# Kernel tuning notes

Measured on AMD Instinct MI355X. Metric: run time of the kernel, lower is better.

The kernel has to match this reference:

```python
import math
import jax, jax.numpy as jnp
import numpy as np

D_MODEL = 128
NUM_HEADS = 8
FACTOR = 5


def setup_inputs() -> dict:
    key = jax.random.key(0)
    ks = jax.random.split(key, 9)
    B, L, dm = 2, 4096, D_MODEL
    s = 1.0 / math.sqrt(dm)
    return {
        "x": jax.random.normal(ks[0], (B, L, dm), dtype=jnp.float32),
        "Wq": jax.random.normal(ks[1], (dm, dm), dtype=jnp.float32) * s,
        "bq": jnp.zeros((dm,), jnp.float32),
        "Wk": jax.random.normal(ks[2], (dm, dm), dtype=jnp.float32) * s,
        "bk": jnp.zeros((dm,), jnp.float32),
        "Wv": jax.random.normal(ks[3], (dm, dm), dtype=jnp.float32) * s,
        "bv": jnp.zeros((dm,), jnp.float32),
        "Wo": jax.random.normal(ks[4], (dm, dm), dtype=jnp.float32) * s,
        "bo": jnp.zeros((dm,), jnp.float32),
    }


def reference(x, Wq, bq, Wk, bk, Wv, bv, Wo, bo):
    B, L, dm = x.shape
    H = NUM_HEADS
    D = dm // H
    inv_sqrt_d = 1.0 / math.sqrt(D)

    def split_heads(t):  # [B,L,dm] -> [B,H,L,D]
        return t.reshape(B, L, H, D).transpose(0, 2, 1, 3)

    Q = split_heads(x @ Wq + bq)
    K = split_heads(x @ Wk + bk)
    V = split_heads(x @ Wv + bv)

    # sample_k = min(L_K, int(log(L_K) * factor)); L is static under jit
    sample_k = min(L, int(math.log(L) * FACTOR))

    # _prob_QK: full scores, per-query stable exp, mean over queries, top-k keys
    scores_full = jnp.einsum("bhqd,bhkd->bhqk", Q, K) * inv_sqrt_d  # [B,H,L,L]
    m = jnp.max(scores_full, axis=-1, keepdims=True)
    e = jnp.exp(scores_full - m)
    mean_attn = jnp.mean(e, axis=2)  # [B,H,L_K]
    _, idx = jax.lax.top_k(mean_attn, sample_k)  # [B,H,sample_k]

    # gather sampled keys/values along the key axis
    Ks = jnp.take_along_axis(K, idx[..., None], axis=2)  # [B,H,s,D]
    Vs = jnp.take_along_axis(V, idx[..., None], axis=2)

    attn = jax.nn.softmax(jnp.einsum("bhqd,bhsd->bhqs", Q, Ks) * inv_sqrt_d, axis=-1)
    out = jnp.einsum("bhqs,bhsd->bhqd", attn, Vs)  # [B,H,L,D]
    out = out.transpose(0, 2, 1, 3).reshape(B, L, dm)
    return out @ Wo + bo
```

## Files before the change

kernel.cpp:

```cpp
#include <hip/hip_runtime.h>
#include <hip/hip_bf16.h>

#define L 4096
#define DM 128
#define NH 8
#define HD 16
#define NBH 16
#define SK 41
#define NSPLIT 8
#define SLICE (L/NSPLIT)
#define KK (SLICE/16)
#define QSCALE 0.36067376022224085f

typedef __attribute__((ext_vector_type(8))) short s16x8;
typedef __attribute__((ext_vector_type(4))) float f32x4;

#define MFMA16(A,B,C) __builtin_amdgcn_mfma_f32_16x16x32_bf16(A,B,C,0,0,0)

__device__ __forceinline__ float bf2f(unsigned short h){ return __uint_as_float(((unsigned)h)<<16); }
__device__ __forceinline__ unsigned short f2bf(float f){
  unsigned u = __float_as_uint(f);
  u += 0x7FFFu + ((u>>16)&1u);
  return (unsigned short)(u>>16);
}
__device__ __forceinline__ float fast_exp2(float x){
  float r;
  asm("v_exp_f32 %0, %1" : "=v"(r) : "v"(x));
  return r;
}

__global__ __launch_bounds__(256) void prep(
    const float* __restrict__ x,
    const float* __restrict__ Wq, const float* __restrict__ Wk,
    const float* __restrict__ Wv, const float* __restrict__ Wo,
    unsigned short* __restrict__ Xh, unsigned short* __restrict__ Xl,
    unsigned short* __restrict__ Wph, unsigned short* __restrict__ Wpl)
{
  const int t = threadIdx.x;
  const int blk = blockIdx.x;
  if (blk < 1024){
    const long base = (long)blk*1024 + t*4;
    float4 v = *(const float4*)(x + base);
    unsigned short h[4], lo[4];
    h[0]=f2bf(v.x); lo[0]=f2bf(v.x - bf2f(h[0]));
    h[1]=f2bf(v.y); lo[1]=f2bf(v.y - bf2f(h[1]));
    h[2]=f2bf(v.z); lo[2]=f2bf(v.z - bf2f(h[2]));
    h[3]=f2bf(v.w); lo[3]=f2bf(v.w - bf2f(h[3]));
    *(uint2*)(Xh+base) = *(uint2*)h;
    *(uint2*)(Xl+base) = *(uint2*)lo;
  } else {
    const int e = (blk-1024)*256 + t;
    const int p = e >> 14;
    const int idx = e & 16383;
    const int j = idx & 7;
    const int f = idx >> 3;
    const int n = f & 127;
    const int kcg = f >> 7;
    const int k = (kcg>>1)*16 + (kcg&1)*8 + j;
    const float* W = (p==0)?Wq:((p==1)?Wk:((p==2)?Wv:Wo));
    const float v = W[k*128 + n];
    const unsigned short h = f2bf(v);
    Wph[e] = h;
    Wpl[e] = f2bf(v - bf2f(h));
  }
}

__global__ __launch_bounds__(256) void proj_mfma(
    const unsigned short* __restrict__ Xh, const unsigned short* __restrict__ Xl,
    const unsigned short* __restrict__ Wph, const unsigned short* __restrict__ Wpl,
    const float* __restrict__ bq, const float* __restrict__ bk, const float* __restrict__ bv,
    unsigned short* __restrict__ Qh, unsigned short* __restrict__ Ql,
    unsigned short* __restrict__ Kh, unsigned short* __restrict__ Kl,
    float* __restrict__ Vo)
{
  const int p = blockIdx.y;
  const float* __restrict__ bias = (p==0)?bq:((p==1)?bk:bv);
  __shared__ __align__(16) unsigned short wh[16384];
  __shared__ __align__(16) unsigned short wl[16384];
  const int t = threadIdx.x;
  {
    const uint4* gh = (const uint4*)(Wph + (long)p*16384);
    const uint4* gl = (const uint4*)(Wpl + (long)p*16384);
    uint4* sh = (uint4*)wh; uint4* sl = (uint4*)wl;
#pragma unroll
    for (int i=0;i<8;++i){ sh[t + i*256] = gh[t + i*256]; sl[t + i*256] = gl[t + i*256]; }
  }
  __syncthreads();
  const int w = t>>6, l = t&63;
  const int lc = l&15, g = l>>4;
  const int mbase = blockIdx.x*128 + w*32;
  f32x4 acc[2][8];
#pragma unroll
  for (int mt=0;mt<2;++mt)
#pragma unroll
    for (int nt=0;nt<8;++nt){ acc[mt][nt][0]=0.f; acc[mt][nt][1]=0.f; acc[mt][nt][2]=0.f; acc[mt][nt][3]=0.f; }
  const unsigned short* __restrict__ Asrc = (g<2)? Xh : Xl;
  const int koff = (g&1)*8;
  for (int kc=0; kc<8; ++kc){
    s16x8 a[2];
#pragma unroll
    for (int mt=0;mt<2;++mt)
      a[mt] = *(const s16x8*)(Asrc + ((long)(mbase + mt*16 + lc))*128 + kc*16 + koff);
#pragma unroll
    for (int nt=0;nt<8;++nt){
      const int fi = (kc*2+(g&1))*128 + nt*16 + lc;
      s16x8 b1 = ((const s16x8*)wh)[fi];
      s16x8 b2 = ((const s16x8*)wl)[fi];
#pragma unroll
      for (int mt=0;mt<2;++mt){
        acc[mt][nt] = MFMA16(a[mt], b1, acc[mt][nt]);
        acc[mt][nt] = MFMA16(a[mt], b2, acc[mt][nt]);
      }
    }
  }
#pragma unroll
  for (int nt=0;nt<8;++nt){
    const float bb = bias[nt*16 + lc];
#pragma unroll
    for (int mt=0;mt<2;++mt){
#pragma unroll
      for (int r=0;r<4;++r){
        const int row = mbase + mt*16 + g*4 + r;
        float v = acc[mt][nt][r] + bb;
        const int b = row>>12, li = row&4095;
        const long o = (((long)(b*NH + nt))*L + li)*HD + lc;
        if (p==2){
          Vo[o] = v;
        } else {
          if (p==0) v *= QSCALE;
          const unsigned short h = f2bf(v);
          const unsigned short lo2 = f2bf(v - bf2f(h));
          if (p==0){ Qh[o]=h; Ql[o]=lo2; } else { Kh[o]=h; Kl[o]=lo2; }
        }
      }
    }
  }
}

__global__ __launch_bounds__(256) void rowmax_k(
    const unsigned short* __restrict__ Qh, const unsigned short* __restrict__ Ql,
    const unsigned short* __restrict__ Kh, const unsigned short* __restrict__ Kl,
    float* __restrict__ mpart)
{
  const int bh = blockIdx.y, qt = blockIdx.x, ks = blockIdx.z;
  const int t = threadIdx.x, w = t>>6, l = t&63;
  const int half = (l>>4)&1, part = l>>5, lc = l&15;
  __shared__ __align__(16) unsigned short khs[SLICE*HD];
  __shared__ __align__(16) unsigned short kls[SLICE*HD];
  {
    const uint4* gh = (const uint4*)(Kh + ((long)bh*L + ks*SLICE)*HD);
    const uint4* gl = (const uint4*)(Kl + ((long)bh*L + ks*SLICE)*HD);
    uint4* sh = (uint4*)khs; uint4* sl = (uint4*)kls;
#pragma unroll
    for (int i=0;i<4;++i){ sh[t + i*256] = gh[t + i*256]; sl[t + i*256] = gl[t + i*256]; }
  }
  s16x8 aq[4];
  {
    const unsigned short* Qsrc = part ? Ql : Qh;
#pragma unroll
    for (int m=0;m<4;++m){
      const int row = qt*256 + w*64 + m*16 + lc;
      aq[m] = *(const s16x8*)(Qsrc + (((long)bh*L + row)*HD) + half*8);
    }
  }
  __syncthreads();
  f32x4 fz; fz[0]=0.f; fz[1]=0.f; fz[2]=0.f; fz[3]=0.f;
  f32x4 rmax[4];
#pragma unroll
  for (int m=0;m<4;++m){ rmax[m][0]=rmax[m][1]=rmax[m][2]=rmax[m][3]=-3.4e38f; }
  const int boff = lc*HD + half*8;
  f32x4 accA[4], accB[4];
  {
    s16x8 b1 = *(const s16x8*)(khs + boff);
    s16x8 b2 = *(const s16x8*)(kls + boff);
#pragma unroll
    for (int m=0;m<4;++m){ accA[m] = MFMA16(aq[m], b2, fz); accA[m] = MFMA16(aq[m], b1, accA[m]); }
  }
  for (int kk=0; kk<KK-2; kk+=2){
    {
      s16x8 b1 = *(const s16x8*)(khs + (kk+1)*256 + boff);
      s16x8 b2 = *(const s16x8*)(kls + (kk+1)*256 + boff);
#pragma unroll
      for (int m=0;m<4;++m){ accB[m] = MFMA16(aq[m], b2, fz); accB[m] = MFMA16(aq[m], b1, accB[m]); }
    }
#pragma unroll
    for (int m=0;m<4;++m)
#pragma unroll
      for (int r=0;r<4;++r) rmax[m][r] = fmaxf(rmax[m][r], accA[m][r]);
    {
      s16x8 b1 = *(const s16x8*)(khs + (kk+2)*256 + boff);
      s16x8 b2 = *(const s16x8*)(kls + (kk+2)*256 + boff);
#pragma unroll
      for (int m=0;m<4;++m){ accA[m] = MFMA16(aq[m], b2, fz); accA[m] = MFMA16(aq[m], b1, accA[m]); }
    }
#pragma unroll
    for (int m=0;m<4;++m)
#pragma unroll
      for (int r=0;r<4;++r) rmax[m][r] = fmaxf(rmax[m][r], accB[m][r]);
  }
  {
    s16x8 b1 = *(const s16x8*)(khs + (KK-1)*256 + boff);
    s16x8 b2 = *(const s16x8*)(kls + (KK-1)*256 + boff);
#pragma unroll
    for (int m=0;m<4;++m){ accB[m] = MFMA16(aq[m], b2, fz); accB[m] = MFMA16(aq[m], b1, accB[m]); }
  }
#pragma unroll
  for (int m=0;m<4;++m)
#pragma unroll
    for (int r=0;r<4;++r) rmax[m][r] = fmaxf(fmaxf(rmax[m][r], accA[m][r]), accB[m][r]);
#pragma unroll
  for (int m=0;m<4;++m){
#pragma unroll
    for (int r=0;r<4;++r){
      float v = rmax[m][r];
      v = fmaxf(v, __shfl_xor(v, 1));
      v = fmaxf(v, __shfl_xor(v, 2));
      v = fmaxf(v, __shfl_xor(v, 4));
      v = fmaxf(v, __shfl_xor(v, 8));
      rmax[m][r] = v;
    }
  }
  if (lc == 0){
    const int q4 = l>>4;
#pragma unroll
    for (int m=0;m<4;++m){
#pragma unroll
      for (int r=0;r<4;++r){
        const int row = qt*256 + w*64 + m*16 + q4*4 + r;
        mpart[((long)ks*NBH + bh)*L + row] = rmax[m][r];
      }
    }
  }
}

__global__ __launch_bounds__(256) void mreduce(
    const float* __restrict__ mpart, float* __restrict__ wq)
{
  const int i = blockIdx.x*256 + threadIdx.x;
  float m = -3.4e38f;
#pragma unroll
  for (int p=0;p<NSPLIT;++p) m = fmaxf(m, mpart[(long)p*NBH*L + i]);
  wq[i] = fast_exp2(-m);
}

__global__ __launch_bounds__(256) void colexp_k(
    const unsigned short* __restrict__ Kh, const unsigned short* __restrict__ Kl,
    const unsigned short* __restrict__ Qh, const unsigned short* __restrict__ Ql,
    const float* __restrict__ wq, float* __restrict__ cspart)
{
  const int bh = blockIdx.y, kt = blockIdx.x, qs = blockIdx.z;
  const int t = threadIdx.x, w = t>>6, l = t&63;
  const int half = (l>>4)&1, part = l>>5, lc = l&15;
  __shared__ __align__(16) unsigned short qhs[SLICE*HD];
  __shared__ __align__(16) unsigned short qls[SLICE*HD];
  __shared__ float ws_s[SLICE];
  {
    const uint4* gh = (const uint4*)(Qh + ((long)bh*L + qs*SLICE)*HD);
    const uint4* gl = (const uint4*)(Ql + ((long)bh*L + qs*SLICE)*HD);
    uint4* sh = (uint4*)qhs; uint4* sl = (uint4*)qls;
#pragma unroll
    for (int i=0;i<4;++i){ sh[t + i*256] = gh[t + i*256]; sl[t + i*256] = gl[t + i*256]; }
    const float* wg = wq + (long)bh*L + qs*SLICE;
    ws_s[t] = wg[t];
    ws_s[t+256] = wg[t+256];
  }
  s16x8 ak[4];
  {
    const unsigned short* Ksrc = part ? Kl : Kh;
#pragma unroll
    for (int m=0;m<4;++m){
      const int key = kt*256 + w*64 + m*16 + lc;
      ak[m] = *(const s16x8*)(Ksrc + (((long)bh*L + key)*HD) + half*8);
    }
  }
  __syncthreads();
  f32x4 fz; fz[0]=0.f; fz[1]=0.f; fz[2]=0.f; fz[3]=0.f;
  f32x4 csum[4];
#pragma unroll
  for (int m=0;m<4;++m){ csum[m][0]=0.f; csum[m][1]=0.f; csum[m][2]=0.f; csum[m][3]=0.f; }
  const int boff = lc*HD + half*8;
  f32x4 accA[4], accB[4];
  {
    s16x8 b1 = *(const s16x8*)(qhs + boff);
    s16x8 b2 = *(const s16x8*)(qls + boff);
#pragma unroll
    for (int m=0;m<4;++m){ accA[m] = MFMA16(ak[m], b2, fz); accA[m] = MFMA16(ak[m], b1, accA[m]); }
  }
  for (int kk=0; kk<KK-2; kk+=2){
    {
      s16x8 b1 = *(const s16x8*)(qhs + (kk+1)*256 + boff);
      s16x8 b2 = *(const s16x8*)(qls + (kk+1)*256 + boff);
#pragma unroll
      for (int m=0;m<4;++m){ accB[m] = MFMA16(ak[m], b2, fz); accB[m] = MFMA16(ak[m], b1, accB[m]); }
    }
    {
      const float cw = ws_s[kk*16 + lc];
#pragma unroll
      for (int m=0;m<4;++m)
#pragma unroll
        for (int r=0;r<4;++r)
          csum[m][r] = fmaf(fast_exp2(accA[m][r]), cw, csum[m][r]);
    }
    {
      s16x8 b1 = *(const s16x8*)(qhs + (kk+2)*256 + boff);
      s16x8 b2 = *(const s16x8*)(qls + (kk+2)*256 + boff);
#pragma unroll
      for (int m=0;m<4;++m){ accA[m] = MFMA16(ak[m], b2, fz); accA[m] = MFMA16(ak[m], b1, accA[m]); }
    }
    {
      const float cw = ws_s[(kk+1)*16 + lc];
#pragma unroll
      for (int m=0;m<4;++m)
#pragma unroll
        for (int r=0;r<4;++r)
          csum[m][r] = fmaf(fast_exp2(accB[m][r]), cw, csum[m][r]);
    }
  }
  {
    s16x8 b1 = *(const s16x8*)(qhs + (KK-1)*256 + boff);
    s16x8 b2 = *(const s16x8*)(qls + (KK-1)*256 + boff);
#pragma unroll
    for (int m=0;m<4;++m){ accB[m] = MFMA16(ak[m], b2, fz); accB[m] = MFMA16(ak[m], b1, accB[m]); }
  }
  {
    const float cwA = ws_s[(KK-2)*16 + lc];
    const float cwB = ws_s[(KK-1)*16 + lc];
#pragma unroll
    for (int m=0;m<4;++m)
#pragma unroll
      for (int r=0;r<4;++r){
        csum[m][r] = fmaf(fast_exp2(accA[m][r]), cwA, csum[m][r]);
        csum[m][r] = fmaf(fast_exp2(accB[m][r]), cwB, csum[m][r]);
      }
  }
#pragma unroll
  for (int m=0;m<4;++m){
#pragma unroll
    for (int r=0;r<4;++r){
      float v = csum[m][r];
      v += __shfl_xor(v, 1);
      v += __shfl_xor(v, 2);
      v += __shfl_xor(v, 4);
      v += __shfl_xor(v, 8);
      csum[m][r] = v;
    }
  }
  if (lc == 0){
    const int k4 = l>>4;
#pragma unroll
    for (int m=0;m<4;++m){
#pragma unroll
      for (int r=0;r<4;++r){
        const int key = kt*256 + w*64 + m*16 + k4*4 + r;
        cspart[((long)qs*NBH + bh)*L + key] = csum[m][r];
      }
    }
  }
}

__global__ __launch_bounds__(256) void topk_gather(
    const float* __restrict__ cspart,
    const unsigned short* __restrict__ Kh, const unsigned short* __restrict__ Kl,
    const float* __restrict__ V,
    float* __restrict__ Ks, float* __restrict__ Vs)
{
  const int bh = blockIdx.x;
  const int t = threadIdx.x;
  __shared__ float vals[4096];
  __shared__ unsigned hist[2048];
  __shared__ unsigned suf[256];
  __shared__ int meta[4];
  __shared__ int sel[SK];
  __shared__ int sorted[SK];
  __shared__ int tiei[4096];

  for (int i=t; i<1024; i+=256){
    float4 s = {0.f,0.f,0.f,0.f};
#pragma unroll
    for (int p=0;p<NSPLIT;++p){
      float4 v = *(const float4*)(cspart + ((long)p*NBH + bh)*L + i*4);
      s.x += v.x; s.y += v.y; s.z += v.z; s.w += v.w;
    }
    *(float4*)&vals[i*4] = s;
  }
  __syncthreads();

  int target = SK;
  unsigned B1 = 0, P2 = 0, T = 0;
#pragma unroll
  for (int pass=0; pass<3; ++pass){
    const int nb = (pass<2) ? 2048 : 1024;
    const int chunk = nb >> 8;
    for (int i=t;i<nb;i+=256) hist[i]=0u;
    __syncthreads();
    for (int i=t;i<4096;i+=256){
      const unsigned u = __float_as_uint(vals[i]);
      bool ok; int bk;
      if (pass==0){ ok = true;              bk = (int)(u>>21); }
      else if (pass==1){ ok = ((u>>21)==B1); bk = (int)((u>>10)&0x7FFu); }
      else { ok = ((u>>10)==P2);            bk = (int)(u&0x3FFu); }
      if (ok) atomicAdd(&hist[bk], 1u);
    }
    __syncthreads();
    {
      unsigned c=0;
#pragma unroll
      for (int b=0;b<8;++b) if (b<chunk) c += hist[t*chunk+b];
      suf[t]=c;
    }
    __syncthreads();
    for (int off=1; off<256; off<<=1){
      unsigned add = (t+off<256)? suf[t+off] : 0u;
      __syncthreads();
      suf[t] += add;
      __syncthreads();
    }
    {
      const unsigned mysuf = suf[t];
      const unsigned nxt = (t==255)?0u:suf[t+1];
      if (mysuf >= (unsigned)target && nxt < (unsigned)target){
        unsigned running = nxt;
        for (int b=t*chunk+chunk-1; b>=t*chunk; --b){
          const unsigned h = hist[b];
          if (running + h >= (unsigned)target){ meta[0]=b; meta[1]=(int)running; break; }
          running += h;
        }
      }
    }
    __syncthreads();
    const unsigned B = (unsigned)meta[0];
    target -= meta[1];
    if (pass==0) B1 = B;
    else if (pass==1) P2 = (B1<<11)|B;
    else T = (P2<<10)|B;
    __syncthreads();
  }
  if (t==0){ meta[2]=0; meta[3]=0; }
  __syncthreads();
  for (int i=t;i<4096;i+=256){
    const unsigned u = __float_as_uint(vals[i]);
    if (u > T){ int p = atomicAdd(&meta[2],1); sel[p]=i; }
    else if (u == T){ int p = atomicAdd(&meta[3],1); tiei[p]=i; }
  }
  __syncthreads();
  const int ngt = meta[2];
  const int ntie = meta[3];
  for (int j=t; j<ntie; j+=256){
    const int x = tiei[j];
    int rk=0;
    for (int k=0;k<ntie;++k) rk += (tiei[k] < x);
    if (rk < target) sel[ngt+rk] = x;
  }
  __syncthreads();
  if (t<SK){
    int x=sel[t]; int rk=0;
    for (int j=0;j<SK;++j) rk += (sel[j]<x);
    sorted[rk]=x;
  }
  __syncthreads();
  for (int i=t;i<SK*HD;i+=256){
    const int j=i>>4, dd=i&15;
    const int key=sorted[j];
    const long src=((long)bh*L+key)*HD+dd;
    Ks[(long)bh*SK*HD+i]=bf2f(Kh[src])+bf2f(Kl[src]);
    Vs[(long)bh*SK*HD+i]=V[src];
  }
}

__global__ __launch_bounds__(256) void sattn(
    const unsigned short* __restrict__ Qh, const unsigned short* __restrict__ Ql,
    const float* __restrict__ Ks, const float* __restrict__ Vs,
    unsigned short* __restrict__ AOh, unsigned short* __restrict__ AOl)
{
  const int bh = blockIdx.y, qb = blockIdx.x;
  const int t = threadIdx.x;
  __shared__ float ks[SK*HD], vs[SK*HD];
  for (int i=t; i<SK*HD; i+=256){
    ks[i] = Ks[(long)bh*SK*HD + i];
    vs[i] = Vs[(long)bh*SK*HD + i];
  }
  __syncthreads();
  const int q = qb*128 + (t>>1);
  const int half = t&1;
  const long qo = ((long)bh*L + q)*HD;
  float qv[16];
  {
    s16x8 h0 = *(const s16x8*)(Qh+qo);
    s16x8 h1 = *(const s16x8*)(Qh+qo+8);
    s16x8 l0 = *(const s16x8*)(Ql+qo);
    s16x8 l1 = *(const s16x8*)(Ql+qo+8);
#pragma unroll
    for (int d=0; d<8; ++d){
      qv[d]   = bf2f((unsigned short)h0[d]) + bf2f((unsigned short)l0[d]);
      qv[d+8] = bf2f((unsigned short)h1[d]) + bf2f((unsigned short)l1[d]);
    }
  }
  float mrun = -3.4e38f, lrun = 0.f, out[16];
#pragma unroll
  for (int d=0; d<16; ++d) out[d] = 0.f;
  for (int j=half; j<SK; j+=2){
    float4 k0 = *(const float4*)&ks[j*HD+0];
    float4 k1 = *(const float4*)&ks[j*HD+4];
    float4 k2 = *(const float4*)&ks[j*HD+8];
    float4 k3 = *(const float4*)&ks[j*HD+12];
    float s = qv[0]*k0.x;
    s = fmaf(qv[1],k0.y,s); s = fmaf(qv[2],k0.z,s); s = fmaf(qv[3],k0.w,s);
    s = fmaf(qv[4],k1.x,s); s = fmaf(qv[5],k1.y,s); s = fmaf(qv[6],k1.z,s); s = fmaf(qv[7],k1.w,s);
    s = fmaf(qv[8],k2.x,s); s = fmaf(qv[9],k2.y,s); s = fmaf(qv[10],k2.z,s); s = fmaf(qv[11],k2.w,s);
    s = fmaf(qv[12],k3.x,s); s = fmaf(qv[13],k3.y,s); s = fmaf(qv[14],k3.z,s); s = fmaf(qv[15],k3.w,s);
    if (s > mrun){
      const float c = fast_exp2(mrun - s);
      lrun *= c;
#pragma unroll
      for (int d=0; d<16; ++d) out[d] *= c;
      mrun = s;
    }
    const float p = fast_exp2(s - mrun);
    lrun += p;
    float4 v0 = *(const float4*)&vs[j*HD+0];
    float4 v1 = *(const float4*)&vs[j*HD+4];
    float4 v2 = *(const float4*)&vs[j*HD+8];
    float4 v3 = *(const float4*)&vs[j*HD+12];
    out[0]=fmaf(p,v0.x,out[0]); out[1]=fmaf(p,v0.y,out[1]); out[2]=fmaf(p,v0.z,out[2]); out[3]=fmaf(p,v0.w,out[3]);
    out[4]=fmaf(p,v1.x,out[4]); out[5]=fmaf(p,v1.y,out[5]); out[6]=fmaf(p,v1.z,out[6]); out[7]=fmaf(p,v1.w,out[7]);
    out[8]=fmaf(p,v2.x,out[8]); out[9]=fmaf(p,v2.y,out[9]); out[10]=fmaf(p,v2.z,out[10]); out[11]=fmaf(p,v2.w,out[11]);
    out[12]=fmaf(p,v3.x,out[12]); out[13]=fmaf(p,v3.y,out[13]); out[14]=fmaf(p,v3.z,out[14]); out[15]=fmaf(p,v3.w,out[15]);
  }
  const float mo = __shfl_xor(mrun, 1);
  const float lo = __shfl_xor(lrun, 1);
  const float mm = fmaxf(mrun, mo);
  const float cs_ = fast_exp2(mrun - mm);
  const float co_ = fast_exp2(mo - mm);
  const float ltot = fmaf(lrun, cs_, lo*co_);
  const float inv = 1.f / ltot;
#pragma unroll
  for (int d=0; d<16; ++d){
    const float ov = __shfl_xor(out[d], 1);
    out[d] = fmaf(out[d]*cs_, inv, ov*co_*inv);
  }
  if (half == 0){
    const int b = bh>>3, h = bh&7;
    const long row = (long)b*L + q;
    unsigned short hv[16], lv[16];
#pragma unroll
    for (int d=0; d<16; ++d){
      const float v = out[d];
      hv[d] = f2bf(v);
      lv[d] = f2bf(v - bf2f(hv[d]));
    }
    unsigned short* oh = AOh + row*DM + h*HD;
    unsigned short* ol = AOl + row*DM + h*HD;
    *(uint4*)(oh)   = *(uint4*)(hv);
    *(uint4*)(oh+8) = *(uint4*)(hv+8);
    *(uint4*)(ol)   = *(uint4*)(lv);
    *(uint4*)(ol+8) = *(uint4*)(lv+8);
  }
}

__global__ __launch_bounds__(256) void outproj_mfma(
    const unsigned short* __restrict__ AOh, const unsigned short* __restrict__ AOl,
    const unsigned short* __restrict__ Wph, const unsigned short* __restrict__ Wpl,
    const float* __restrict__ bo, float* __restrict__ out)
{
  __shared__ __align__(16) unsigned short wh[16384];
  __shared__ __align__(16) unsigned short wl[16384];
  const int t = threadIdx.x;
  {
    const uint4* gh = (const uint4*)(Wph + (long)3*16384);
    const uint4* gl = (const uint4*)(Wpl + (long)3*16384);
    uint4* sh = (uint4*)wh; uint4* sl = (uint4*)wl;
#pragma unroll
    for (int i=0;i<8;++i){ sh[t + i*256] = gh[t + i*256]; sl[t + i*256] = gl[t + i*256]; }
  }
  __syncthreads();
  const int w = t>>6, l = t&63;
  const int lc = l&15, g = l>>4;
  const int mbase = blockIdx.x*128 + w*32;
  f32x4 acc[2][8];
#pragma unroll
  for (int mt=0;mt<2;++mt)
#pragma unroll
    for (int nt=0;nt<8;++nt){ acc[mt][nt][0]=0.f; acc[mt][nt][1]=0.f; acc[mt][nt][2]=0.f; acc[mt][nt][3]=0.f; }
  const unsigned short* __restrict__ Asrc = (g<2)? AOh : AOl;
  const int koff = (g&1)*8;
  for (int kc=0; kc<8; ++kc){
    s16x8 a[2];
#pragma unroll
    for (int mt=0;mt<2;++mt)
      a[mt] = *(const s16x8*)(Asrc + ((long)(mbase + mt*16 + lc))*128 + kc*16 + koff);
#pragma unroll
    for (int nt=0;nt<8;++nt){
      const int fi = (kc*2+(g&1))*128 + nt*16 + lc;
      s16x8 b1 = ((const s16x8*)wh)[fi];
      s16x8 b2 = ((const s16x8*)wl)[fi];
#pragma unroll
      for (int mt=0;mt<2;++mt){
        acc[mt][nt] = MFMA16(a[mt], b1, acc[mt][nt]);
        acc[mt][nt] = MFMA16(a[mt], b2, acc[mt][nt]);
      }
    }
  }
#pragma unroll
  for (int nt=0;nt<8;++nt){
    const float bb = bo[nt*16 + lc];
#pragma unroll
    for (int mt=0;mt<2;++mt){
#pragma unroll
      for (int r=0;r<4;++r){
        const int row = mbase + mt*16 + g*4 + r;
        out[(long)row*DM + nt*16 + lc] = acc[mt][nt][r] + bb;
      }
    }
  }
}

extern "C" void kernel_launch(void* const* d_in, const int* in_sizes, int n_in,
                              void* d_out, int out_size, void* d_ws, size_t ws_size,
                              hipStream_t stream)
{
  const float* x  = (const float*)d_in[0];
  const float* Wq = (const float*)d_in[1];
  const float* bq = (const float*)d_in[2];
  const float* Wk = (const float*)d_in[3];
  const float* bk = (const float*)d_in[4];
  const float* Wv = (const float*)d_in[5];
  const float* bv = (const float*)d_in[6];
  const float* Wo = (const float*)d_in[7];
  const float* bo = (const float*)d_in[8];
  float* out = (float*)d_out;

  char* wsp = (char*)d_ws;
  size_t o = 0;
  auto alloc = [&](size_t bytes)->char*{
    char* p = wsp + o; o += (bytes + 255) & ~(size_t)255; return p;
  };
  unsigned short* Qh = (unsigned short*)alloc((size_t)NBH*L*HD*2);
  unsigned short* Ql = (unsigned short*)alloc((size_t)NBH*L*HD*2);
  unsigned short* Kh = (unsigned short*)alloc((size_t)NBH*L*HD*2);
  unsigned short* Kl = (unsigned short*)alloc((size_t)NBH*L*HD*2);
  float* Vv    = (float*)alloc((size_t)NBH*L*HD*4);
  float* mpart = (float*)alloc((size_t)NSPLIT*NBH*L*4);
  float* cspart= (float*)alloc((size_t)NSPLIT*NBH*L*4);
  float* wqv   = (float*)alloc((size_t)NBH*L*4);
  float* Ks    = (float*)alloc((size_t)NBH*SK*HD*4);
  float* Vs    = (float*)alloc((size_t)NBH*SK*HD*4);
  unsigned short* Xh  = (unsigned short*)alloc((size_t)2*L*DM*2);
  unsigned short* Xl  = (unsigned short*)alloc((size_t)2*L*DM*2);
  unsigned short* AOh = (unsigned short*)alloc((size_t)2*L*DM*2);
  unsigned short* AOl = (unsigned short*)alloc((size_t)2*L*DM*2);
  unsigned short* Wph = (unsigned short*)alloc((size_t)4*16384*2);
  unsigned short* Wpl = (unsigned short*)alloc((size_t)4*16384*2);

  prep<<<1280,256,0,stream>>>(x,Wq,Wk,Wv,Wo,Xh,Xl,Wph,Wpl);
  proj_mfma<<<dim3(64,3),256,0,stream>>>(Xh,Xl,Wph,Wpl,bq,bk,bv,Qh,Ql,Kh,Kl,Vv);
  rowmax_k<<<dim3(16,16,NSPLIT),256,0,stream>>>(Qh,Ql,Kh,Kl,mpart);
  mreduce<<<NBH*L/256,256,0,stream>>>(mpart,wqv);
  colexp_k<<<dim3(16,16,NSPLIT),256,0,stream>>>(Kh,Kl,Qh,Ql,wqv,cspart);
  topk_gather<<<16,256,0,stream>>>(cspart,Kh,Kl,Vv,Ks,Vs);
  sattn<<<dim3(32,16),256,0,stream>>>(Qh,Ql,Ks,Vs,AOh,AOl);
  outproj_mfma<<<64,256,0,stream>>>(AOh,AOl,Wph,Wpl,bo,out);
}
```

Measured before the change: 137.8 us.

## Halve GEMM tiles, fuse max-reduce into colexp, two-pass softmax in sampled attention

The projection and output-projection GEMMs now give each wave 16 rows instead of 32, which doubles the grid from 64 to 128 blocks so more of the GPU is occupied, at the cost of loading the weights into LDS twice as often. The separate mreduce kernel is removed. colexp_k now reduces the per-split row maxima itself while loading its slice, which saves one launch and one intermediate buffer, though each colexp block repeats that reduction. The sampled-attention kernel replaces its online softmax with a branch-free two-pass version: it keeps all 21 scores in registers, takes the max, then accumulates. This uses more registers.

After: 132.1 us, median of 2. -4.1%, faster.

```diff
diff --git a/kernel.cpp b/kernel.cpp
--- a/kernel.cpp
+++ b/kernel.cpp
@@ -88,50 +88,39 @@
   __syncthreads();
   const int w = t>>6, l = t&63;
   const int lc = l&15, g = l>>4;
-  const int mbase = blockIdx.x*128 + w*32;
-  f32x4 acc[2][8];
-#pragma unroll
-  for (int mt=0;mt<2;++mt)
-#pragma unroll
-    for (int nt=0;nt<8;++nt){ acc[mt][nt][0]=0.f; acc[mt][nt][1]=0.f; acc[mt][nt][2]=0.f; acc[mt][nt][3]=0.f; }
+  const int mbase = blockIdx.x*64 + w*16;
+  f32x4 acc[8];
+#pragma unroll
+  for (int nt=0;nt<8;++nt){ acc[nt][0]=0.f; acc[nt][1]=0.f; acc[nt][2]=0.f; acc[nt][3]=0.f; }
   const unsigned short* __restrict__ Asrc = (g<2)? Xh : Xl;
   const int koff = (g&1)*8;
   for (int kc=0; kc<8; ++kc){
-    s16x8 a[2];
-#pragma unroll
-    for (int mt=0;mt<2;++mt)
-      a[mt] = *(const s16x8*)(Asrc + ((long)(mbase + mt*16 + lc))*128 + kc*16 + koff);
+    s16x8 a = *(const s16x8*)(Asrc + ((long)(mbase + lc))*128 + kc*16 + koff);
 #pragma unroll
     for (int nt=0;nt<8;++nt){
       const int fi = (kc*2+(g&1))*128 + nt*16 + lc;
       s16x8 b1 = ((const s16x8*)wh)[fi];
       s16x8 b2 = ((const s16x8*)wl)[fi];
-#pragma unroll
-      for (int mt=0;mt<2;++mt){
-        acc[mt][nt] = MFMA16(a[mt], b1, acc[mt][nt]);
-        acc[mt][nt] = MFMA16(a[mt], b2, acc[mt][nt]);
-      }
+      acc[nt] = MFMA16(a, b1, acc[nt]);
+      acc[nt] = MFMA16(a, b2, acc[nt]);
     }
   }
 #pragma unroll
   for (int nt=0;nt<8;++nt){
     const float bb = bias[nt*16 + lc];
 #pragma unroll
-    for (int mt=0;mt<2;++mt){
-#pragma unroll
-      for (int r=0;r<4;++r){
-        const int row = mbase + mt*16 + g*4 + r;
-        float v = acc[mt][nt][r] + bb;
-        const int b = row>>12, li = row&4095;
-        const long o = (((long)(b*NH + nt))*L + li)*HD + lc;
-        if (p==2){
-          Vo[o] = v;
-        } else {
-          if (p==0) v *= QSCALE;
-          const unsigned short h = f2bf(v);
-          const unsigned short lo2 = f2bf(v - bf2f(h));
-          if (p==0){ Qh[o]=h; Ql[o]=lo2; } else { Kh[o]=h; Kl[o]=lo2; }
-        }
+    for (int r=0;r<4;++r){
+      const int row = mbase + g*4 + r;
+      float v = acc[nt][r] + bb;
+      const int b = row>>12, li = row&4095;
+      const long o = (((long)(b*NH + nt))*L + li)*HD + lc;
+      if (p==2){
+        Vo[o] = v;
+      } else {
+        if (p==0) v *= QSCALE;
+        const unsigned short h = f2bf(v);
+        const unsigned short lo2 = f2bf(v - bf2f(h));
+        if (p==0){ Qh[o]=h; Ql[o]=lo2; } else { Kh[o]=h; Kl[o]=lo2; }
       }
     }
   }
@@ -233,20 +222,10 @@
   }
 }
 
-__global__ __launch_bounds__(256) void mreduce(
-    const float* __restrict__ mpart, float* __restrict__ wq)
-{
-  const int i = blockIdx.x*256 + threadIdx.x;
-  float m = -3.4e38f;
-#pragma unroll
-  for (int p=0;p<NSPLIT;++p) m = fmaxf(m, mpart[(long)p*NBH*L + i]);
-  wq[i] = fast_exp2(-m);
-}
-
 __global__ __launch_bounds__(256) void colexp_k(
     const unsigned short* __restrict__ Kh, const unsigned short* __restrict__ Kl,
     const unsigned short* __restrict__ Qh, const unsigned short* __restrict__ Ql,
-    const float* __restrict__ wq, float* __restrict__ cspart)
+    const float* __restrict__ mpart, float* __restrict__ cspart)
 {
   const int bh = blockIdx.y, kt = blockIdx.x, qs = blockIdx.z;
   const int t = threadIdx.x, w = t>>6, l = t&63;
@@ -260,9 +239,15 @@
     uint4* sh = (uint4*)qhs; uint4* sl = (uint4*)qls;
 #pragma unroll
     for (int i=0;i<4;++i){ sh[t + i*256] = gh[t + i*256]; sl[t + i*256] = gl[t + i*256]; }
-    const float* wg = wq + (long)bh*L + qs*SLICE;
-    ws_s[t] = wg[t];
-    ws_s[t+256] = wg[t+256];
+#pragma unroll
+    for (int rr=0; rr<2; ++rr){
+      const int tq = t + rr*256;
+      const long qi = (long)bh*L + qs*SLICE + tq;
+      float m = -3.4e38f;
+#pragma unroll
+      for (int p=0;p<NSPLIT;++p) m = fmaxf(m, mpart[(long)p*NBH*L + qi]);
+      ws_s[tq] = fast_exp2(-m);
+    }
   }
   s16x8 ak[4];
   {
@@ -495,41 +480,51 @@
       qv[d+8] = bf2f((unsigned short)h1[d]) + bf2f((unsigned short)l1[d]);
     }
   }
-  float mrun = -3.4e38f, lrun = 0.f, out[16];
+  float sc[21];
+#pragma unroll
+  for (int i=0;i<21;++i){
+    const int j = half + 2*i;
+    if (j < SK){
+      float4 k0 = *(const float4*)&ks[j*HD+0];
+      float4 k1 = *(const float4*)&ks[j*HD+4];
+      float4 k2 = *(const float4*)&ks[j*HD+8];
+      float4 k3 = *(const float4*)&ks[j*HD+12];
+      float s = qv[0]*k0.x;
+      s = fmaf(qv[1],k0.y,s); s = fmaf(qv[2],k0.z,s); s = fmaf(qv[3],k0.w,s);
+      s = fmaf(qv[4],k1.x,s); s = fmaf(qv[5],k1.y,s); s = fmaf(qv[6],k1.z,s); s = fmaf(qv[7],k1.w,s);
+      s = fmaf(qv[8],k2.x,s); s = fmaf(qv[9],k2.y,s); s = fmaf(qv[10],k2.z,s); s = fmaf(qv[11],k2.w,s);
+      s = fmaf(qv[12],k3.x,s); s = fmaf(qv[13],k3.y,s); s = fmaf(qv[14],k3.z,s); s = fmaf(qv[15],k3.w,s);
+      sc[i] = s;
+    } else {
+      sc[i] = -3.4e38f;
+    }
+  }
+  float m = sc[0];
+#pragma unroll
+  for (int i=1;i<21;++i) m = fmaxf(m, sc[i]);
+  float lrun = 0.f, out[16];
 #pragma unroll
   for (int d=0; d<16; ++d) out[d] = 0.f;
-  for (int j=half; j<SK; j+=2){
-    float4 k0 = *(const float4*)&ks[j*HD+0];
-    float4 k1 = *(const float4*)&ks[j*HD+4];
-    float4 k2 = *(const float4*)&ks[j*HD+8];
-    float4 k3 = *(const float4*)&ks[j*HD+12];
-    float s = qv[0]*k0.x;
-    s = fmaf(qv[1],k0.y,s); s = fmaf(qv[2],k0.z,s); s = fmaf(qv[3],k0.w,s);
-    s = fmaf(qv[4],k1.x,s); s = fmaf(qv[5],k1.y,s); s = fmaf(qv[6],k1.z,s); s = fmaf(qv[7],k1.w,s);
-    s = fmaf(qv[8],k2.x,s); s = fmaf(qv[9],k2.y,s); s = fmaf(qv[10],k2.z,s); s = fmaf(qv[11],k2.w,s);
-    s = fmaf(qv[12],k3.x,s); s = fmaf(qv[13],k3.y,s); s = fmaf(qv[14],k3.z,s); s = fmaf(qv[15],k3.w,s);
-    if (s > mrun){
-      const float c = fast_exp2(mrun - s);
-      lrun *= c;
-#pragma unroll
-      for (int d=0; d<16; ++d) out[d] *= c;
-      mrun = s;
-    }
-    const float p = fast_exp2(s - mrun);
+#pragma unroll
+  for (int i=0;i<21;++i){
+    const int j = half + 2*i;
+    const float p = fast_exp2(sc[i] - m);
     lrun += p;
-    float4 v0 = *(const float4*)&vs[j*HD+0];
-    float4 v1 = *(const float4*)&vs[j*HD+4];
-    float4 v2 = *(const float4*)&vs[j*HD+8];
-    float4 v3 = *(const float4*)&vs[j*HD+12];
-    out[0]=fmaf(p,v0.x,out[0]); out[1]=fmaf(p,v0.y,out[1]); out[2]=fmaf(p,v0.z,out[2]); out[3]=fmaf(p,v0.w,out[3]);
-    out[4]=fmaf(p,v1.x,out[4]); out[5]=fmaf(p,v1.y,out[5]); out[6]=fmaf(p,v1.z,out[6]); out[7]=fmaf(p,v1.w,out[7]);
-    out[8]=fmaf(p,v2.x,out[8]); out[9]=fmaf(p,v2.y,out[9]); out[10]=fmaf(p,v2.z,out[10]); out[11]=fmaf(p,v2.w,out[11]);
-    out[12]=fmaf(p,v3.x,out[12]); out[13]=fmaf(p,v3.y,out[13]); out[14]=fmaf(p,v3.z,out[14]); out[15]=fmaf(p,v3.w,out[15]);
-  }
-  const float mo = __shfl_xor(mrun, 1);
+    if (j < SK){
+      float4 v0 = *(const float4*)&vs[j*HD+0];
+      float4 v1 = *(const float4*)&vs[j*HD+4];
+      float4 v2 = *(const float4*)&vs[j*HD+8];
+      float4 v3 = *(const float4*)&vs[j*HD+12];
+      out[0]=fmaf(p,v0.x,out[0]); out[1]=fmaf(p,v0.y,out[1]); out[2]=fmaf(p,v0.z,out[2]); out[3]=fmaf(p,v0.w,out[3]);
+      out[4]=fmaf(p,v1.x,out[4]); out[5]=fmaf(p,v1.y,out[5]); out[6]=fmaf(p,v1.z,out[6]); out[7]=fmaf(p,v1.w,out[7]);
+      out[8]=fmaf(p,v2.x,out[8]); out[9]=fmaf(p,v2.y,out[9]); out[10]=fmaf(p,v2.z,out[10]); out[11]=fmaf(p,v2.w,out[11]);
+      out[12]=fmaf(p,v3.x,out[12]); out[13]=fmaf(p,v3.y,out[13]); out[14]=fmaf(p,v3.z,out[14]); out[15]=fmaf(p,v3.w,out[15]);
+    }
+  }
+  const float mo = __shfl_xor(m, 1);
   const float lo = __shfl_xor(lrun, 1);
-  const float mm = fmaxf(mrun, mo);
-  const float cs_ = fast_exp2(mrun - mm);
+  const float mm = fmaxf(m, mo);
+  const float cs_ = fast_exp2(m - mm);
   const float co_ = fast_exp2(mo - mm);
   const float ltot = fmaf(lrun, cs_, lo*co_);
   const float inv = 1.f / ltot;
@@ -575,41 +570,30 @@
   __syncthreads();
   const int w = t>>6, l = t&63;
   const int lc = l&15, g = l>>4;
-  const int mbase = blockIdx.x*128 + w*32;
-  f32x4 acc[2][8];
-#pragma unroll
-  for (int mt=0;mt<2;++mt)
-#pragma unroll
-    for (int nt=0;nt<8;++nt){ acc[mt][nt][0]=0.f; acc[mt][nt][1]=0.f; acc[mt][nt][2]=0.f; acc[mt][nt][3]=0.f; }
+  const int mbase = blockIdx.x*64 + w*16;
+  f32x4 acc[8];
+#pragma unroll
+  for (int nt=0;nt<8;++nt){ acc[nt][0]=0.f; acc[nt][1]=0.f; acc[nt][2]=0.f; acc[nt][3]=0.f; }
   const unsigned short* __restrict__ Asrc = (g<2)? AOh : AOl;
   const int koff = (g&1)*8;
   for (int kc=0; kc<8; ++kc){
-    s16x8 a[2];
-#pragma unroll
-    for (int mt=0;mt<2;++mt)
-      a[mt] = *(const s16x8*)(Asrc + ((long)(mbase + mt*16 + lc))*128 + kc*16 + koff);
+    s16x8 a = *(const s16x8*)(Asrc + ((long)(mbase + lc))*128 + kc*16 + koff);
 #pragma unroll
     for (int nt=0;nt<8;++nt){
       const int fi = (kc*2+(g&1))*128 + nt*16 + lc;
       s16x8 b1 = ((const s16x8*)wh)[fi];
       s16x8 b2 = ((const s16x8*)wl)[fi];
-#pragma unroll
-      for (int mt=0;mt<2;++mt){
-        acc[mt][nt] = MFMA16(a[mt], b1, acc[mt][nt]);
-        acc[mt][nt] = MFMA16(a[mt], b2, acc[mt][nt]);
-      }
+      acc[nt] = MFMA16(a, b1, acc[nt]);
+      acc[nt] = MFMA16(a, b2, acc[nt]);
     }
   }
 #pragma unroll
   for (int nt=0;nt<8;++nt){
     const float bb = bo[nt*16 + lc];
 #pragma unroll
-    for (int mt=0;mt<2;++mt){
-#pragma unroll
-      for (int r=0;r<4;++r){
-        const int row = mbase + mt*16 + g*4 + r;
-        out[(long)row*DM + nt*16 + lc] = acc[mt][nt][r] + bb;
-      }
+    for (int r=0;r<4;++r){
+      const int row = mbase + g*4 + r;
+      out[(long)row*DM + nt*16 + lc] = acc[nt][r] + bb;
     }
   }
 }
@@ -641,7 +625,6 @@
   float* Vv    = (float*)alloc((size_t)NBH*L*HD*4);
   float* mpart = (float*)alloc((size_t)NSPLIT*NBH*L*4);
   float* cspart= (float*)alloc((size_t)NSPLIT*NBH*L*4);
-  float* wqv   = (float*)alloc((size_t)NBH*L*4);
   float* Ks    = (float*)alloc((size_t)NBH*SK*HD*4);
   float* Vs    = (float*)alloc((size_t)NBH*SK*HD*4);
   unsigned short* Xh  = (unsigned short*)alloc((size_t)2*L*DM*2);
@@ -652,11 +635,10 @@
   unsigned short* Wpl = (unsigned short*)alloc((size_t)4*16384*2);
 
   prep<<<1280,256,0,stream>>>(x,Wq,Wk,Wv,Wo,Xh,Xl,Wph,Wpl);
-  proj_mfma<<<dim3(64,3),256,0,stream>>>(Xh,Xl,Wph,Wpl,bq,bk,bv,Qh,Ql,Kh,Kl,Vv);
+  proj_mfma<<<dim3(128,3),256,0,stream>>>(Xh,Xl,Wph,Wpl,bq,bk,bv,Qh,Ql,Kh,Kl,Vv);
   rowmax_k<<<dim3(16,16,NSPLIT),256,0,stream>>>(Qh,Ql,Kh,Kl,mpart);
-  mreduce<<<NBH*L/256,256,0,stream>>>(mpart,wqv);
-  colexp_k<<<dim3(16,16,NSPLIT),256,0,stream>>>(Kh,Kl,Qh,Ql,wqv,cspart);
+  colexp_k<<<dim3(16,16,NSPLIT),256,0,stream>>>(Kh,Kl,Qh,Ql,mpart,cspart);
   topk_gather<<<16,256,0,stream>>>(cspart,Kh,Kl,Vv,Ks,Vs);
   sattn<<<dim3(32,16),256,0,stream>>>(Qh,Ql,Ks,Vs,AOh,AOl);
-  outproj_mfma<<<64,256,0,stream>>>(AOh,AOl,Wph,Wpl,bo,out);
-}
+  outproj_mfma<<<128,256,0,stream>>>(AOh,AOl,Wph,Wpl,bo,out);
+}
```
